# Performance work log

Measured on AMD Instinct MI355X. Metric: run time of the kernel, lower is better.

Reference implementation:

```python
import jax, jax.numpy as jnp
import numpy as np

N_NODES = 646  # fixed by nn.LayerNorm([646, 64])
LN_EPS = 1e-5


def gcn_conv(x, edge_index, W, b):
    """PyG GCNConv: out = D^-1/2 (A+I) D^-1/2 (x W) + b, scatter-add at target."""
    n = x.shape[0]
    h = x @ W  # [N, out_dim]
    loop = jnp.arange(n, dtype=edge_index.dtype)
    row = jnp.concatenate([edge_index[0], loop])  # source
    col = jnp.concatenate([edge_index[1], loop])  # target
    deg = jax.ops.segment_sum(jnp.ones_like(col, dtype=h.dtype), col, num_segments=n)
    dinv = jnp.where(deg > 0, jax.lax.rsqrt(deg), 0.0)
    norm = dinv[row] * dinv[col]  # [E+N]
    out = jax.ops.segment_sum(h[row] * norm[:, None], col, num_segments=n)
    return out + b


def setup_inputs() -> dict:
    key = jax.random.key(0)
    ks = jax.random.split(key, 8)
    F, H, L, E = 32768, 64, 128, 646 * 64
    x = jax.random.normal(ks[0], (N_NODES, F), dtype=jnp.float32)
    edge_index = jax.random.randint(ks[1], (2, E), 0, N_NODES, dtype=jnp.int64)
    s = 1.0 / np.sqrt(F)
    W1 = jax.random.normal(ks[2], (F, H), dtype=jnp.float32) * s
    b1 = jax.random.normal(ks[3], (H,), dtype=jnp.float32) * 0.01
    W2 = jax.random.normal(ks[4], (H, L), dtype=jnp.float32) * (1.0 / np.sqrt(H))
    b2 = jax.random.normal(ks[5], (L,), dtype=jnp.float32) * 0.01
    LPw = jax.random.normal(ks[6], (F, H), dtype=jnp.float32) * s
    LPb = jax.random.normal(ks[7], (H,), dtype=jnp.float32) * 0.01
    return {"x": x, "edge_index": edge_index, "W1": W1, "b1": b1,
            "W2": W2, "b2": b2, "LPw": LPw, "LPb": LPb}


def reference(x, edge_index, W1, b1, W2, b2, LPw, LPb):
    res = x @ LPw + LPb                       # Linear residual branch [N, 64]
    h = gcn_conv(x, edge_index, W1, b1)       # GCN1 [N, 64]
    h = res + h
    h = h * jax.nn.sigmoid(h)                 # SiLU
    # LayerNorm over BOTH dims [646, 64], no affine (elementwise_affine=False)
    mu = jnp.mean(h)
    var = jnp.mean(jnp.square(h - mu))
    h = (h - mu) * jax.lax.rsqrt(var + LN_EPS)
    out = gcn_conv(h, edge_index, W2, b2)     # GCN2 [N, num_label]
    return out
```

## Files before the change

### kernel.cpp

```cpp
#include <hip/hip_runtime.h>
#include <hip/hip_bf16.h>

#define NN 646
#define FF 32768
#define HH 64
#define LL 128
#define TOT (NN*HH)
#define OUTTOT (NN*LL)
#define WT_STRIDE (FF + 32)
#define KSPLIT 64
#define KSLICE (FF / KSPLIT)
#define BK 32
#define NSTEP (KSLICE / BK)
#define NGEMM (21 * KSPLIT)

typedef float f32x4 __attribute__((ext_vector_type(4)));
typedef short short8 __attribute__((ext_vector_type(8)));

__device__ __forceinline__ unsigned short f2bf(float f) {
  __hip_bfloat16 h = __float2bfloat16(f);
  return __builtin_bit_cast(unsigned short, h);
}
__device__ __forceinline__ short8 pack8(float4 u, float4 v) {
  short8 r;
  r[0] = (short)f2bf(u.x); r[1] = (short)f2bf(u.y);
  r[2] = (short)f2bf(u.z); r[3] = (short)f2bf(u.w);
  r[4] = (short)f2bf(v.x); r[5] = (short)f2bf(v.y);
  r[6] = (short)f2bf(v.z); r[7] = (short)f2bf(v.w);
  return r;
}
__device__ __forceinline__ void gload16(const void* g, void* l) {
  __builtin_amdgcn_global_load_lds(
      (const __attribute__((address_space(1))) void*)g,
      (__attribute__((address_space(3))) void*)l, 16, 0, 0);
}
__device__ __forceinline__ bool probe_i64(const int* e32, int* orr) {
  if (threadIdx.x == 0) *orr = 0;
  __syncthreads();
  if (threadIdx.x < 256 && e32[2 * threadIdx.x + 1] != 0) atomicOr(orr, 1);
  __syncthreads();
  return *orr == 0;
}

__global__ __launch_bounds__(1024) void k_zero(int* __restrict__ cnt,
                                               float* __restrict__ stats) {
  int t = threadIdx.x;
  if (t < NN) cnt[t] = 0;
  if (t < 2) stats[t] = 0.f;
}

__global__ __launch_bounds__(256) void k_init(const float* __restrict__ W1,
                                              const float* __restrict__ LPw,
                                              unsigned short* __restrict__ wt,
                                              const int* __restrict__ e32, int E,
                                              int* __restrict__ cnt,
                                              const float* __restrict__ W2,
                                              float* __restrict__ cs) {
  if (blockIdx.x < 512) {
    __shared__ float t[64][129];
    int k0 = blockIdx.x * 64;
    for (int idx = threadIdx.x; idx < 64 * 128; idx += 256) {
      int kk = idx >> 7, n = idx & 127;
      float v = (n < 64) ? W1[(size_t)(k0 + kk) * 64 + n]
                         : LPw[(size_t)(k0 + kk) * 64 + (n - 64)];
      t[kk][n] = v;
    }
    __syncthreads();
    for (int idx = threadIdx.x; idx < 1024; idx += 256) {
      int n = idx >> 3;
      int kc = (idx & 7) * 8;
      short8 v;
#pragma unroll
      for (int u = 0; u < 8; ++u) v[u] = (short)f2bf(t[kc + u][n]);
      *reinterpret_cast<short8*>(&wt[(size_t)n * WT_STRIDE + k0 + kc]) = v;
    }
    return;
  }
  if (blockIdx.x == 576) {
    __shared__ float r2[2][128];
    int j = threadIdx.x & 127, h = threadIdx.x >> 7;
    float a = 0.f;
    for (int k = h * 32; k < h * 32 + 32; ++k) a += W2[k * LL + j];
    r2[h][j] = a;
    __syncthreads();
    if (h == 0) cs[j] = r2[0][j] + r2[1][j];
    return;
  }
  __shared__ int orr;
  bool i64 = probe_i64(e32, &orr);
  const int* cp = i64 ? (e32 + 2 * (size_t)E) : (e32 + E);
  int st = i64 ? 2 : 1;
  int wid = (blockIdx.x - 512) * 256 + threadIdx.x;
  for (int e = wid; e < E; e += 64 * 256)
    atomicAdd(&cnt[cp[(size_t)e * st]], 1);
}

__global__ __launch_bounds__(256, 6) void k_gemm(const float* __restrict__ x,
                                                 const unsigned short* __restrict__ wt,
                                                 float* __restrict__ partial,
                                                 const int* __restrict__ cnt, int E,
                                                 int* __restrict__ offsets,
                                                 float* __restrict__ dinv,
                                                 int* __restrict__ cursor) {
  __shared__ __align__(16) float As[2][32 * BK];
  __shared__ __align__(16) unsigned short Bs[2][128 * BK];

  int p = blockIdx.x;
  if (p == NGEMM) {
    __shared__ int wtot[4];
    int tid = threadIdx.x;
    int b = 3 * tid;
    int c0 = (b < NN) ? cnt[b] : 0;
    int c1 = (b + 1 < NN) ? cnt[b + 1] : 0;
    int c2 = (b + 2 < NN) ? cnt[b + 2] : 0;
    int s = c0 + c1 + c2;
    int lane = tid & 63, wv = tid >> 6;
    int run = s;
#pragma unroll
    for (int o = 1; o < 64; o <<= 1) { int v = __shfl_up(run, o); if (lane >= o) run += v; }
    if (lane == 63) wtot[wv] = run;
    __syncthreads();
    int wbase = 0;
    for (int i = 0; i < wv; ++i) wbase += wtot[i];
    int excl = wbase + run - s;
    if (b < NN)     { offsets[b]     = excl;           cursor[b]     = excl;           dinv[b]     = rsqrtf((float)(c0 + 1)); }
    if (b + 1 < NN) { offsets[b + 1] = excl + c0;      cursor[b + 1] = excl + c0;      dinv[b + 1] = rsqrtf((float)(c1 + 1)); }
    if (b + 2 < NN) { offsets[b + 2] = excl + c0 + c1; cursor[b + 2] = excl + c0 + c1; dinv[b + 2] = rsqrtf((float)(c2 + 1)); }
    if (tid == 0) offsets[NN] = E;
    return;
  }

  int xcd = p & 7, idx = p >> 3;
  int ks = xcd + 8 * (idx / 21);
  int mt = idx % 21;
  int tid = threadIdx.x;
  int w = tid >> 6, l = tid & 63;
  int lr = l & 15, g = l >> 4;
  int mh = w & 1, nh = w >> 1;
  int ksbase = ks * KSLICE;

  f32x4 acc0 = {0.f, 0.f, 0.f, 0.f}, acc1 = acc0, acc2 = acc0, acc3 = acc0;
  int arow = mh * 16 + lr, arm = arow & 7;

  int a_row = tid >> 3, a_cc = tid & 7;
  int a_c = a_cc ^ (a_row & 7);
  int a_rowg = mt * 32 + a_row; if (a_rowg > NN - 1) a_rowg = NN - 1;
  const float* a_src0 = x + (size_t)a_rowg * FF + ksbase + a_c * 4;

  auto STAGE = [&](int buf, int step) {
    int kb = step * BK;
    gload16(a_src0 + kb, (char*)(&As[buf][0]) + tid * 16);
#pragma unroll
    for (int j = 0; j < 2; ++j) {
      int pp = j * 256 + tid;
      int row = pp >> 2, cc = pp & 3;
      int c = cc ^ (row & 3);
      gload16(wt + (size_t)row * WT_STRIDE + ksbase + kb + c * 8,
              (char*)(&Bs[buf][0]) + pp * 16);
    }
  };

  auto COMPUTE = [&](int buf) {
    const char* Ab = (const char*)(&As[buf][0]);
    const char* Bb = (const char*)(&Bs[buf][0]);
    int c0 = g * 2, c1 = g * 2 + 1;
    float4 lo = *(const float4*)(Ab + (arow * 8 + (c0 ^ arm)) * 16);
    float4 hi = *(const float4*)(Ab + (arow * 8 + (c1 ^ arm)) * 16);
    short8 af = pack8(lo, hi);
#pragma unroll
    for (int nf = 0; nf < 4; ++nf) {
      int brow = nh * 64 + nf * 16 + lr;
      short8 b = *(const short8*)(Bb + (brow * 4 + (g ^ (brow & 3))) * 16);
      f32x4* ac = (nf == 0) ? &acc0 : (nf == 1) ? &acc1 : (nf == 2) ? &acc2 : &acc3;
      *ac = __builtin_amdgcn_mfma_f32_16x16x32_bf16(af, b, *ac, 0, 0, 0);
    }
  };

  STAGE(0, 0);
  STAGE(1, 1);
#pragma unroll
  for (int t = 0; t < NSTEP; ++t) {
    if (t + 1 < NSTEP) {
      asm volatile("s_waitcnt vmcnt(3)" ::: "memory");
    } else {
      asm volatile("s_waitcnt vmcnt(0)" ::: "memory");
    }
    __builtin_amdgcn_s_barrier();
    COMPUTE(t & 1);
    if (t + 2 < NSTEP) {
      __builtin_amdgcn_s_barrier();
      STAGE(t & 1, t + 2);
    }
  }

  float* pp = partial + (size_t)ks * OUTTOT;
  int colb = nh * 64 + lr;
#pragma unroll
  for (int j = 0; j < 4; ++j) {
    int m = mt * 32 + mh * 16 + g * 4 + j;
    if (m < NN) {
      pp[m * LL + colb]      = acc0[j];
      pp[m * LL + colb + 16] = acc1[j];
      pp[m * LL + colb + 32] = acc2[j];
      pp[m * LL + colb + 48] = acc3[j];
    }
  }
}

__global__ __launch_bounds__(256) void k_redplace(const float* __restrict__ partial,
                                                  const float* __restrict__ LPb,
                                                  float* __restrict__ hcat,
                                                  const int* __restrict__ e32, int E,
                                                  int* __restrict__ cursor,
                                                  int* __restrict__ srcs) {
  if (blockIdx.x < 81) {
    int i4 = blockIdx.x * 256 + threadIdx.x;
    if (i4 * 4 >= OUTTOT) return;
    f32x4 s = {0.f, 0.f, 0.f, 0.f};
#pragma unroll 8
    for (int ks = 0; ks < KSPLIT; ++ks)
      s += *reinterpret_cast<const f32x4*>(partial + (size_t)ks * OUTTOT + i4 * 4);
    int n = (i4 * 4) & 127;
    if (n & 64) s += *reinterpret_cast<const f32x4*>(LPb + (n - 64));
    *reinterpret_cast<f32x4*>(hcat + i4 * 4) = s;
    return;
  }
  __shared__ int orr;
  bool i64 = probe_i64(e32, &orr);
  int e = (blockIdx.x - 81) * 256 + threadIdx.x;
  if (e >= E) return;
  const int* rp = e32;
  const int* cp = i64 ? (e32 + 2 * (size_t)E) : (e32 + E);
  int st = i64 ? 2 : 1;
  int r = rp[(size_t)e * st];
  int c = cp[(size_t)e * st];
  int pos = atomicAdd(&cursor[c], 1);
  srcs[pos] = r;
}

__global__ __launch_bounds__(256) void k_fuse1(const int* __restrict__ offs,
                                               const int* __restrict__ srcs,
                                               const float* __restrict__ dinv,
                                               const float* __restrict__ hcat,
                                               const float* __restrict__ b1,
                                               const float* __restrict__ W2,
                                               float* __restrict__ hwr,
                                               float* __restrict__ sdi,
                                               float* __restrict__ stats) {
  int c = blockIdx.x;
  int j = threadIdx.x & 63, qt = threadIdx.x >> 6;
  int o0 = offs[c], o1 = offs[c + 1];
  float acc = 0.f, sd = 0.f;
  for (int i = o0 + qt; i < o1; i += 4) {
    int r = srcs[i];
    float dr = dinv[r];
    acc += hcat[r * LL + j] * dr;
    sd += dr;
  }
  __shared__ float red[4][64];
  __shared__ float sdl[4];
  __shared__ float hnl[64];
  red[qt][j] = acc;
  if (j == 0) sdl[qt] = sd;
  __syncthreads();
  if (qt == 0) {
    float di = dinv[c];
    float gb = (red[0][j] + red[1][j] + red[2][j] + red[3][j]) * di;
    float t = hcat[c * LL + 64 + j] + b1[j] + gb + hcat[c * LL + j] * di * di;
    float s = t / (1.f + __expf(-t));
    hnl[j] = s;
    float sum = s, sq = s * s;
#pragma unroll
    for (int o = 32; o; o >>= 1) { sum += __shfl_down(sum, o); sq += __shfl_down(sq, o); }
    if (j == 0) {
      atomicAdd(&stats[0], sum);
      atomicAdd(&stats[1], sq);
      sdi[c] = sdl[0] + sdl[1] + sdl[2] + sdl[3] + di;
    }
  }
  __syncthreads();
  int j2 = threadIdx.x & 127, h = threadIdx.x >> 7;
  float a2 = 0.f;
#pragma unroll
  for (int k = h * 32; k < h * 32 + 32; ++k) a2 += hnl[k] * W2[k * LL + j2];
  __shared__ float r2[2][128];
  r2[h][j2] = a2;
  __syncthreads();
  if (h == 0) hwr[c * LL + j2] = (r2[0][j2] + r2[1][j2]) * dinv[c];
}

__global__ __launch_bounds__(256) void k_fuse2(const int* __restrict__ offs,
                                               const int* __restrict__ srcs,
                                               const float* __restrict__ dinv,
                                               const float* __restrict__ hwr,
                                               const float* __restrict__ b2,
                                               const float* __restrict__ cs,
                                               const float* __restrict__ sdi,
                                               const float* __restrict__ stats,
                                               float* __restrict__ out) {
  int c = blockIdx.x;
  int j = threadIdx.x & 127, hf = threadIdx.x >> 7;
  int o0 = offs[c], o1 = offs[c + 1];
  float acc = 0.f;
  for (int i = o0 + hf; i < o1; i += 2) acc += hwr[srcs[i] * LL + j];
  __shared__ float red[2][128];
  red[hf][j] = acc;
  __syncthreads();
  if (hf == 0) {
    float mu = stats[0] * (1.f / TOT);
    float var = stats[1] * (1.f / TOT) - mu * mu;
    float rs = rsqrtf(var + 1e-5f);
    float S = red[0][j] + red[1][j] + hwr[c * LL + j];
    out[c * LL + j] = b2[j] + dinv[c] * (rs * S - rs * mu * cs[j] * sdi[c]);
  }
}

extern "C" void kernel_launch(void* const* d_in, const int* in_sizes, int n_in,
                              void* d_out, int out_size, void* d_ws, size_t ws_size,
                              hipStream_t stream) {
  const float* x   = (const float*)d_in[0];
  const int*   e32 = (const int*)d_in[1];
  const float* W1  = (const float*)d_in[2];
  const float* b1  = (const float*)d_in[3];
  const float* W2  = (const float*)d_in[4];
  const float* b2  = (const float*)d_in[5];
  const float* LPw = (const float*)d_in[6];
  const float* LPb = (const float*)d_in[7];
  int E = in_sizes[1] / 2;
  float* out = (float*)d_out;

  char* ws = (char*)d_ws;
  size_t o_wt      = 0;
  size_t o_partial = 8396800;
  size_t o_hcat    = o_partial + (size_t)KSPLIT * OUTTOT * 4;
  size_t o_hwr     = o_hcat + 330752;
  size_t o_dinv    = o_hwr + 330752;
  size_t o_offs    = o_dinv + 2816;
  size_t o_cnt     = o_offs + 2816;
  size_t o_stat    = o_cnt + 2816;
  size_t o_cur     = o_stat + 256;
  size_t o_srcs    = o_cur + 2816;
  size_t o_cs      = o_srcs + 165376;
  size_t o_sdi     = o_cs + 512;

  unsigned short* wt = (unsigned short*)(ws + o_wt);
  float* partial = (float*)(ws + o_partial);
  float* hcat    = (float*)(ws + o_hcat);
  float* hwr     = (float*)(ws + o_hwr);
  float* dinv    = (float*)(ws + o_dinv);
  int*   offs    = (int*)(ws + o_offs);
  int*   cnt     = (int*)(ws + o_cnt);
  float* stats   = (float*)(ws + o_stat);
  int*   cursor  = (int*)(ws + o_cur);
  int*   srcs    = (int*)(ws + o_srcs);
  float* cs      = (float*)(ws + o_cs);
  float* sdi     = (float*)(ws + o_sdi);

  k_zero<<<1, 1024, 0, stream>>>(cnt, stats);
  k_init<<<577, 256, 0, stream>>>(W1, LPw, wt, e32, E, cnt, W2, cs);
  k_gemm<<<NGEMM + 1, 256, 0, stream>>>(x, wt, partial, cnt, E, offs, dinv, cursor);
  k_redplace<<<243, 256, 0, stream>>>(partial, LPb, hcat, e32, E, cursor, srcs);
  k_fuse1<<<NN, 256, 0, stream>>>(offs, srcs, dinv, hcat, b1, W2, hwr, sdi, stats);
  k_fuse2<<<NN, 256, 0, stream>>>(offs, srcs, dinv, hwr, b2, cs, sdi, stats, out);
}
```

Baseline: 99.58 us.

## Enlarge GEMM M-tile to 128 rows so each block reuses weight tiles

The split-K GEMM block tile grows from 32x128 to 128x128. Each wave now computes a 32x128 sub-tile with 16 accumulators, so every staged bf16 weight tile is reused across four times as many rows of x, and the launch drops from 21 to 6 M-tiles per K-slice. This cuts redundant weight loads and LDS B-reads per MFMA. In exchange it raises LDS and register use (occupancy hint lowered from 6 to 3), pads the last M-tile with 122 wasted rows, and reduces the grid to 384 GEMM blocks, which may underfill the GPU.

```diff
diff --git a/kernel.cpp b/kernel.cpp
--- a/kernel.cpp
+++ b/kernel.cpp
@@ -12,7 +12,8 @@
 #define KSLICE (FF / KSPLIT)
 #define BK 32
 #define NSTEP (KSLICE / BK)
-#define NGEMM (21 * KSPLIT)
+#define NMT 6
+#define NGEMM (NMT * KSPLIT)
 
 typedef float f32x4 __attribute__((ext_vector_type(4)));
 typedef short short8 __attribute__((ext_vector_type(8)));
@@ -95,14 +96,14 @@
     atomicAdd(&cnt[cp[(size_t)e * st]], 1);
 }
 
-__global__ __launch_bounds__(256, 6) void k_gemm(const float* __restrict__ x,
+__global__ __launch_bounds__(256, 3) void k_gemm(const float* __restrict__ x,
                                                  const unsigned short* __restrict__ wt,
                                                  float* __restrict__ partial,
                                                  const int* __restrict__ cnt, int E,
                                                  int* __restrict__ offsets,
                                                  float* __restrict__ dinv,
                                                  int* __restrict__ cursor) {
-  __shared__ __align__(16) float As[2][32 * BK];
+  __shared__ __align__(16) float As[2][128 * BK];
   __shared__ __align__(16) unsigned short Bs[2][128 * BK];
 
   int p = blockIdx.x;
@@ -131,31 +132,36 @@
   }
 
   int xcd = p & 7, idx = p >> 3;
-  int ks = xcd + 8 * (idx / 21);
-  int mt = idx % 21;
+  int ks = xcd + 8 * (idx / NMT);
+  int mt = idx % NMT;
   int tid = threadIdx.x;
   int w = tid >> 6, l = tid & 63;
   int lr = l & 15, g = l >> 4;
-  int mh = w & 1, nh = w >> 1;
+  int wr = w * 32;
   int ksbase = ks * KSLICE;
 
-  f32x4 acc0 = {0.f, 0.f, 0.f, 0.f}, acc1 = acc0, acc2 = acc0, acc3 = acc0;
-  int arow = mh * 16 + lr, arm = arow & 7;
-
-  int a_row = tid >> 3, a_cc = tid & 7;
-  int a_c = a_cc ^ (a_row & 7);
-  int a_rowg = mt * 32 + a_row; if (a_rowg > NN - 1) a_rowg = NN - 1;
-  const float* a_src0 = x + (size_t)a_rowg * FF + ksbase + a_c * 4;
+  f32x4 acc[2][8];
+#pragma unroll
+  for (int i = 0; i < 2; ++i)
+#pragma unroll
+    for (int j = 0; j < 8; ++j) acc[i][j] = (f32x4){0.f, 0.f, 0.f, 0.f};
 
   auto STAGE = [&](int buf, int step) {
-    int kb = step * BK;
-    gload16(a_src0 + kb, (char*)(&As[buf][0]) + tid * 16);
+    int kb = ksbase + step * BK;
+#pragma unroll
+    for (int j = 0; j < 4; ++j) {
+      int pp = j * 256 + tid;
+      int row = pp >> 3, cc = pp & 7;
+      int c = cc ^ (row & 7);
+      int rowg = mt * 128 + row; if (rowg > NN - 1) rowg = NN - 1;
+      gload16(x + (size_t)rowg * FF + kb + c * 4, (char*)(&As[buf][0]) + pp * 16);
+    }
 #pragma unroll
     for (int j = 0; j < 2; ++j) {
       int pp = j * 256 + tid;
       int row = pp >> 2, cc = pp & 3;
       int c = cc ^ (row & 3);
-      gload16(wt + (size_t)row * WT_STRIDE + ksbase + kb + c * 8,
+      gload16(wt + (size_t)row * WT_STRIDE + kb + c * 8,
               (char*)(&Bs[buf][0]) + pp * 16);
     }
   };
@@ -163,16 +169,25 @@
   auto COMPUTE = [&](int buf) {
     const char* Ab = (const char*)(&As[buf][0]);
     const char* Bb = (const char*)(&Bs[buf][0]);
-    int c0 = g * 2, c1 = g * 2 + 1;
-    float4 lo = *(const float4*)(Ab + (arow * 8 + (c0 ^ arm)) * 16);
-    float4 hi = *(const float4*)(Ab + (arow * 8 + (c1 ^ arm)) * 16);
-    short8 af = pack8(lo, hi);
-#pragma unroll
-    for (int nf = 0; nf < 4; ++nf) {
-      int brow = nh * 64 + nf * 16 + lr;
+    short8 af0, af1;
+    {
+      int row = wr + lr, rm = row & 7;
+      float4 lo = *(const float4*)(Ab + (row * 8 + ((g * 2) ^ rm)) * 16);
+      float4 hi = *(const float4*)(Ab + (row * 8 + ((g * 2 + 1) ^ rm)) * 16);
+      af0 = pack8(lo, hi);
+    }
+    {
+      int row = wr + 16 + lr, rm = row & 7;
+      float4 lo = *(const float4*)(Ab + (row * 8 + ((g * 2) ^ rm)) * 16);
+      float4 hi = *(const float4*)(Ab + (row * 8 + ((g * 2 + 1) ^ rm)) * 16);
+      af1 = pack8(lo, hi);
+    }
+#pragma unroll
+    for (int nf = 0; nf < 8; ++nf) {
+      int brow = nf * 16 + lr;
       short8 b = *(const short8*)(Bb + (brow * 4 + (g ^ (brow & 3))) * 16);
-      f32x4* ac = (nf == 0) ? &acc0 : (nf == 1) ? &acc1 : (nf == 2) ? &acc2 : &acc3;
-      *ac = __builtin_amdgcn_mfma_f32_16x16x32_bf16(af, b, *ac, 0, 0, 0);
+      acc[0][nf] = __builtin_amdgcn_mfma_f32_16x16x32_bf16(af0, b, acc[0][nf], 0, 0, 0);
+      acc[1][nf] = __builtin_amdgcn_mfma_f32_16x16x32_bf16(af1, b, acc[1][nf], 0, 0, 0);
     }
   };
 
@@ -181,7 +196,7 @@
 #pragma unroll
   for (int t = 0; t < NSTEP; ++t) {
     if (t + 1 < NSTEP) {
-      asm volatile("s_waitcnt vmcnt(3)" ::: "memory");
+      asm volatile("s_waitcnt vmcnt(6)" ::: "memory");
     } else {
       asm volatile("s_waitcnt vmcnt(0)" ::: "memory");
     }
@@ -194,15 +209,15 @@
   }
 
   float* pp = partial + (size_t)ks * OUTTOT;
-  int colb = nh * 64 + lr;
-#pragma unroll
-  for (int j = 0; j < 4; ++j) {
-    int m = mt * 32 + mh * 16 + g * 4 + j;
-    if (m < NN) {
-      pp[m * LL + colb]      = acc0[j];
-      pp[m * LL + colb + 16] = acc1[j];
-      pp[m * LL + colb + 32] = acc2[j];
-      pp[m * LL + colb + 48] = acc3[j];
+#pragma unroll
+  for (int mf = 0; mf < 2; ++mf) {
+#pragma unroll
+    for (int nf = 0; nf < 8; ++nf) {
+#pragma unroll
+      for (int j = 0; j < 4; ++j) {
+        int m = mt * 128 + wr + mf * 16 + g * 4 + j;
+        if (m < NN) pp[m * LL + nf * 16 + lr] = acc[mf][nf][j];
+      }
     }
   }
 }
```

Result: faster. 94.20 us (-5.4%).
